# Optimization experiments

Hardware: AMD Instinct MI355X
Metric: run time of the kernel (lower is better)

Reference implementation:

```python
import jax, jax.numpy as jnp
import numpy as np

B, S, D, DF, H, L, K, NT, NM, MAXD = 16, 128, 384, 1536, 2, 6, 3, 128, 80, 8
LOUT = S * MAXD  # fixed (jit-static) upper bound on expanded mel length


def layer_norm(x, g, b):
    m = x.mean(-1, keepdims=True)
    v = x.var(-1, keepdims=True)
    return (x - m) * jax.lax.rsqrt(v + 1e-5) * g + b


def conv1d_same(x, w, b):
    # x: [B,T,Cin], w: [Cout,Cin,K] (torch Conv1d layout), padding='same'
    y = jax.lax.conv_general_dilated(x.transpose(0, 2, 1), w, (1,), 'SAME',
                                     dimension_numbers=('NCH', 'OIH', 'NCH'))
    return y.transpose(0, 2, 1) + b


def self_attention(x, qkv_w, qkv_b, ow, ob):
    b, t, d = x.shape
    dh = d // H
    qkv = x @ qkv_w + qkv_b
    q, k, v = jnp.split(qkv, 3, axis=-1)
    q = q.reshape(b, t, H, dh)
    k = k.reshape(b, t, H, dh)
    v = v.reshape(b, t, H, dh)
    s = jnp.einsum('bqhd,bkhd->bhqk', q, k) / np.sqrt(dh).astype(x.dtype)
    a = jax.nn.softmax(s, axis=-1)
    o = jnp.einsum('bhqk,bkhd->bqhd', a, v).reshape(b, t, d)
    return o @ ow + ob


def fft_block(x, p):
    qkv_w, qkv_b, ow, ob, g1, b1, c1w, c1b, c2w, c2b, g2, b2 = p
    x = layer_norm(x + self_attention(x, qkv_w, qkv_b, ow, ob), g1, b1)
    h = jax.nn.relu(conv1d_same(x, c1w, c1b))
    h = conv1d_same(h, c2w, c2b)
    return layer_norm(x + h, g2, b2)


def pos_encoding(x):
    t, d = x.shape[1], x.shape[2]
    pos = jnp.arange(t, dtype=x.dtype)[:, None]
    i = jnp.arange(d // 2, dtype=x.dtype)[None, :]
    ang = pos / jnp.power(jnp.asarray(10000.0, x.dtype), 2 * i / d)
    pe = jnp.stack([jnp.sin(ang), jnp.cos(ang)], axis=-1).reshape(t, d)
    return x + pe


def fastspeech_fwd(x, y, emb,
                   ph_qkv_w, ph_qkv_b, ph_out_w, ph_out_b, ph_ln1_g, ph_ln1_b,
                   ph_c1_w, ph_c1_b, ph_c2_w, ph_c2_b, ph_ln2_g, ph_ln2_b,
                   mel_qkv_w, mel_qkv_b, mel_out_w, mel_out_b, mel_ln1_g, mel_ln1_b,
                   mel_c1_w, mel_c1_b, mel_c2_w, mel_c2_b, mel_ln2_g, mel_ln2_b,
                   dp_c1_w, dp_c1_b, dp_ln1_g, dp_ln1_b, dp_c2_w, dp_c2_b,
                   dp_ln2_g, dp_ln2_b, dp_lin_w, dp_lin_b,
                   proj_w, proj_b):
    h = emb[x]                      # [B,S,D]
    h = pos_encoding(h)
    ph = (ph_qkv_w, ph_qkv_b, ph_out_w, ph_out_b, ph_ln1_g, ph_ln1_b,
          ph_c1_w, ph_c1_b, ph_c2_w, ph_c2_b, ph_ln2_g, ph_ln2_b)
    for i in range(L):
        h = fft_block(h, tuple(a[i] for a in ph))

    # duration predictor (teacher durations y are used for expansion)
    dp = jax.nn.relu(conv1d_same(h, dp_c1_w, dp_c1_b))
    dp = layer_norm(dp, dp_ln1_g, dp_ln1_b)
    dp = jax.nn.relu(conv1d_same(dp, dp_c2_w, dp_c2_b))
    dp = layer_norm(dp, dp_ln2_g, dp_ln2_b)
    _pred_lengths = (dp @ dp_lin_w + dp_lin_b)[..., 0]  # [B,S] (used only for MSE loss)

    # length regulation: repeat_interleave + pad, vectorized via cumsum+searchsorted
    ends = jnp.cumsum(y, axis=1)                        # [B,S]
    grid = jnp.arange(LOUT)
    idx = jax.vmap(lambda e: jnp.searchsorted(e, grid, side='right'))(ends)  # [B,LOUT]
    idx = jnp.minimum(idx, S - 1)
    mask = grid[None, :] < ends[:, -1:]                 # valid (non-pad) positions
    h = jnp.take_along_axis(h, idx[..., None], axis=1) * mask[..., None]  # [B,LOUT,D]

    mel = (mel_qkv_w, mel_qkv_b, mel_out_w, mel_out_b, mel_ln1_g, mel_ln1_b,
           mel_c1_w, mel_c1_b, mel_c2_w, mel_c2_b, mel_ln2_g, mel_ln2_b)
    for i in range(L):
        h = fft_block(h, tuple(a[i] for a in mel))

    return h @ proj_w + proj_b                          # [B,LOUT,n_mels]


def setup_inputs() -> dict:
    key = jax.random.key(0)
    ks = iter(jax.random.split(key, 64))
    sc = 0.02
    d = {}
    d['x'] = jax.random.randint(next(ks), (B, S), 0, NT, dtype=jnp.int64)
    d['y'] = jax.random.randint(next(ks), (B, S), 1, MAXD + 1, dtype=jnp.int32)
    d['emb'] = jax.random.normal(next(ks), (NT, D), jnp.float32) * sc
    for p in ('ph', 'mel'):
        d[p + '_qkv_w'] = jax.random.normal(next(ks), (L, D, 3 * D), jnp.float32) * sc
        d[p + '_qkv_b'] = jnp.zeros((L, 3 * D), jnp.float32)
        d[p + '_out_w'] = jax.random.normal(next(ks), (L, D, D), jnp.float32) * sc
        d[p + '_out_b'] = jnp.zeros((L, D), jnp.float32)
        d[p + '_ln1_g'] = jnp.ones((L, D), jnp.float32)
        d[p + '_ln1_b'] = jnp.zeros((L, D), jnp.float32)
        d[p + '_c1_w'] = jax.random.normal(next(ks), (L, DF, D, K), jnp.float32) * sc
        d[p + '_c1_b'] = jnp.zeros((L, DF), jnp.float32)
        d[p + '_c2_w'] = jax.random.normal(next(ks), (L, D, DF, K), jnp.float32) * sc
        d[p + '_c2_b'] = jnp.zeros((L, D), jnp.float32)
        d[p + '_ln2_g'] = jnp.ones((L, D), jnp.float32)
        d[p + '_ln2_b'] = jnp.zeros((L, D), jnp.float32)
    d['dp_c1_w'] = jax.random.normal(next(ks), (D, D, K), jnp.float32) * sc
    d['dp_c1_b'] = jnp.zeros((D,), jnp.float32)
    d['dp_ln1_g'] = jnp.ones((D,), jnp.float32)
    d['dp_ln1_b'] = jnp.zeros((D,), jnp.float32)
    d['dp_c2_w'] = jax.random.normal(next(ks), (D, D, K), jnp.float32) * sc
    d['dp_c2_b'] = jnp.zeros((D,), jnp.float32)
    d['dp_ln2_g'] = jnp.ones((D,), jnp.float32)
    d['dp_ln2_b'] = jnp.zeros((D,), jnp.float32)
    d['dp_lin_w'] = jax.random.normal(next(ks), (D, 1), jnp.float32) * sc
    d['dp_lin_b'] = jnp.zeros((1,), jnp.float32)
    d['proj_w'] = jax.random.normal(next(ks), (D, NM), jnp.float32) * sc
    d['proj_b'] = jnp.zeros((NM,), jnp.float32)
    return d


def reference(x, y, emb,
              ph_qkv_w, ph_qkv_b, ph_out_w, ph_out_b, ph_ln1_g, ph_ln1_b,
              ph_c1_w, ph_c1_b, ph_c2_w, ph_c2_b, ph_ln2_g, ph_ln2_b,
              mel_qkv_w, mel_qkv_b, mel_out_w, mel_out_b, mel_ln1_g, mel_ln1_b,
              mel_c1_w, mel_c1_b, mel_c2_w, mel_c2_b, mel_ln2_g, mel_ln2_b,
              dp_c1_w, dp_c1_b, dp_ln1_g, dp_ln1_b, dp_c2_w, dp_c2_b,
              dp_ln2_g, dp_ln2_b, dp_lin_w, dp_lin_b,
              proj_w, proj_b):
    return fastspeech_fwd(x, y, emb,
                          ph_qkv_w, ph_qkv_b, ph_out_w, ph_out_b, ph_ln1_g, ph_ln1_b,
                          ph_c1_w, ph_c1_b, ph_c2_w, ph_c2_b, ph_ln2_g, ph_ln2_b,
                          mel_qkv_w, mel_qkv_b, mel_out_w, mel_out_b, mel_ln1_g, mel_ln1_b,
                          mel_c1_w, mel_c1_b, mel_c2_w, mel_c2_b, mel_ln2_g, mel_ln2_b,
                          dp_c1_w, dp_c1_b, dp_ln1_g, dp_ln1_b, dp_c2_w, dp_c2_b,
                          dp_ln2_g, dp_ln2_b, dp_lin_w, dp_lin_b,
                          proj_w, proj_b)
```

## Files before the change

kernel.cpp:

```cpp
#include <hip/hip_runtime.h>
#include <cstddef>
#include <cmath>

constexpr int CB  = 16;
constexpr int CS  = 128;
constexpr int CD  = 384;
constexpr int CDF = 1536;
constexpr int CH  = 2;
constexpr int CL  = 6;
constexpr int CNM = 80;
constexpr int CLOUT = 1024;
constexpr int CDH = 192;

typedef __bf16 bf16x8 __attribute__((ext_vector_type(8)));
typedef float  f32x4  __attribute__((ext_vector_type(4)));

constexpr int LDT = 72;
__global__ __launch_bounds__(256) void mm_bf16(
    const __bf16* __restrict__ A, long lda, long sA1, long sA2,
    const __bf16* __restrict__ Bt, long ldb, long sB1, long sB2,
    const float* __restrict__ bias, const float* __restrict__ resid,
    void* __restrict__ Cp, long ldc, long sC1, long sC2,
    int M, int N, int K, int zdiv, int relu, int outBf, float scale)
{
    int z = blockIdx.z;
    int zb = z / zdiv, zh = z % zdiv;
    const __bf16* Ab = A  + (long)zb * sA1 + (long)zh * sA2;
    const __bf16* Bb = Bt + (long)zb * sB1 + (long)zh * sB2;
    long coff = (long)zb * sC1 + (long)zh * sC2;

    __shared__ __attribute__((aligned(16))) __bf16 As[128 * LDT];
    __shared__ __attribute__((aligned(16))) __bf16 Bs[128 * LDT];

    int tid  = threadIdx.x;
    int lane = tid & 63;
    int wave = tid >> 6;
    int quad = lane >> 4;
    int l16  = lane & 15;
    int wm = (wave >> 1) * 64;
    int wn = (wave & 1) * 64;

    int mBase = blockIdx.y * 128;
    int nBase = blockIdx.x * 128;

    int trow  = tid >> 3;
    int tcol8 = (tid & 7) * 8;

    f32x4 acc[4][4] = {};

    for (int k0 = 0; k0 < K; k0 += 64) {
#pragma unroll
        for (int p = 0; p < 4; ++p) {
            int r = p * 32 + trow;
            const __bf16* ga = Ab + (long)(mBase + r) * lda + k0 + tcol8;
            *(uint4*)(&As[r * LDT + tcol8]) = *(const uint4*)ga;
            int gn = nBase + r; gn = gn < N ? gn : N - 1;
            const __bf16* gb = Bb + (long)gn * ldb + k0 + tcol8;
            *(uint4*)(&Bs[r * LDT + tcol8]) = *(const uint4*)gb;
        }
        __syncthreads();
#pragma unroll
        for (int ks = 0; ks < 2; ++ks) {
            int kof = ks * 32 + quad * 8;
            bf16x8 af[4], bfr[4];
#pragma unroll
            for (int mt = 0; mt < 4; ++mt)
                af[mt] = *(const bf16x8*)(&As[(wm + mt * 16 + l16) * LDT + kof]);
#pragma unroll
            for (int nt = 0; nt < 4; ++nt)
                bfr[nt] = *(const bf16x8*)(&Bs[(wn + nt * 16 + l16) * LDT + kof]);
#pragma unroll
            for (int mt = 0; mt < 4; ++mt)
#pragma unroll
                for (int nt = 0; nt < 4; ++nt)
                    acc[mt][nt] = __builtin_amdgcn_mfma_f32_16x16x32_bf16(
                        af[mt], bfr[nt], acc[mt][nt], 0, 0, 0);
        }
        __syncthreads();
    }

#pragma unroll
    for (int mt = 0; mt < 4; ++mt) {
#pragma unroll
        for (int nt = 0; nt < 4; ++nt) {
            int col = nBase + wn + nt * 16 + l16;
            if (col >= N) continue;
            int row0 = mBase + wm + mt * 16 + quad * 4;
            float bv = bias ? bias[col] : 0.f;
#pragma unroll
            for (int r = 0; r < 4; ++r) {
                long off = coff + (long)(row0 + r) * ldc + col;
                float v = acc[mt][nt][r] * scale + bv;
                if (resid) v += resid[off];
                if (relu) v = fmaxf(v, 0.f);
                if (outBf) ((__bf16*)Cp)[off] = (__bf16)v;
                else       ((float*)Cp)[off] = v;
            }
        }
    }
}

template<int WN>
__global__ __launch_bounds__(256) void conv_mfma2(
    const __bf16* __restrict__ Apad, const __bf16* __restrict__ W,
    const float* __restrict__ bias, const float* __restrict__ resid,
    void* __restrict__ Cp, long ldc, long sC1,
    int T, int Tp2, int Cc, int O, int relu, int outBf)
{
    constexpr int BN   = 2 * WN;
    constexpr int NT   = WN / 16;
    constexpr int LDT2 = 40;

    int z = blockIdx.z;
    int t0 = blockIdx.y * 128;
    int nBase = blockIdx.x * BN;
    const __bf16* Ab = Apad + ((long)z * Tp2 + t0) * Cc;

    __shared__ __attribute__((aligned(16))) __bf16 As[130 * LDT2];
    __shared__ __attribute__((aligned(16))) __bf16 Bs[3][BN * LDT2];

    int tid  = threadIdx.x;
    int lane = tid & 63;
    int wave = tid >> 6;
    int quad = lane >> 4;
    int l16  = lane & 15;
    int wm = (wave >> 1) * 64;
    int wn = (wave & 1) * WN;

    f32x4 acc[4][NT] = {};

    long ldw = 3L * Cc;
    for (int c0 = 0; c0 < Cc; c0 += 32) {
        __syncthreads();
#pragma unroll
        for (int i = 0; i < 3; ++i) {
            int u = tid + i * 256;
            if (u < 520) {
                int r = u >> 2, cc = (u & 3) * 8;
                *(uint4*)(&As[r * LDT2 + cc]) = *(const uint4*)(Ab + (long)r * Cc + c0 + cc);
            }
        }
#pragma unroll
        for (int i = 0; i < 3 * BN / 64; ++i) {
            int u = tid + i * 256;
            int kk = u / (BN * 4), rr = (u >> 2) & (BN - 1), cc = (u & 3) * 8;
            *(uint4*)(&Bs[kk][rr * LDT2 + cc]) =
                *(const uint4*)(W + (long)(nBase + rr) * ldw + kk * Cc + c0 + cc);
        }
        __syncthreads();
#pragma unroll
        for (int kk = 0; kk < 3; ++kk) {
            bf16x8 a[4], b[NT];
#pragma unroll
            for (int mt = 0; mt < 4; ++mt)
                a[mt] = *(const bf16x8*)(&As[(wm + mt * 16 + l16 + kk) * LDT2 + quad * 8]);
#pragma unroll
            for (int nt = 0; nt < NT; ++nt)
                b[nt] = *(const bf16x8*)(&Bs[kk][(wn + nt * 16 + l16) * LDT2 + quad * 8]);
#pragma unroll
            for (int mt = 0; mt < 4; ++mt)
#pragma unroll
                for (int nt = 0; nt < NT; ++nt)
                    acc[mt][nt] = __builtin_amdgcn_mfma_f32_16x16x32_bf16(
                        a[mt], b[nt], acc[mt][nt], 0, 0, 0);
        }
    }

#pragma unroll
    for (int mt = 0; mt < 4; ++mt) {
#pragma unroll
        for (int nt = 0; nt < NT; ++nt) {
            int col = nBase + wn + nt * 16 + l16;
            int trow = t0 + wm + mt * 16 + quad * 4;
            float bv = bias[col];
#pragma unroll
            for (int r = 0; r < 4; ++r) {
                long off = (long)z * sC1 + (long)(trow + r) * ldc + col;
                float v = acc[mt][nt][r] + bv;
                if (resid) v += resid[off];
                if (relu) v = fmaxf(v, 0.f);
                if (outBf) ((__bf16*)Cp)[off] = (__bf16)v;
                else       ((float*)Cp)[off] = v;
            }
        }
    }
}

__global__ __launch_bounds__(512) void flash_attn(
    const __bf16* __restrict__ qkv, __bf16* __restrict__ o, int T, float scl)
{
    int z = blockIdx.y;
    int b = z >> 1, h = z & 1;
    const __bf16* base = qkv + (long)b * T * 3 * CD + h * CDH;
    int qBase = blockIdx.x * 128;

    __shared__ __attribute__((aligned(16))) __bf16 Qs[128][200];
    __shared__ __attribute__((aligned(16))) __bf16 Ks[64][200];
    __shared__ __attribute__((aligned(16))) __bf16 Vt[192][72];
    __shared__ __attribute__((aligned(16))) __bf16 Ps[128][72];

    int tid  = threadIdx.x;
    int lane = tid & 63;
    int wave = tid >> 6;
    int quad = lane >> 4;
    int l16  = lane & 15;
    int wq   = wave * 16;

#pragma unroll
    for (int i = 0; i < 6; ++i) {
        int u = tid + i * 512;
        int r = u / 24, c = (u % 24) * 8;
        *(uint4*)(&Qs[r][c]) = *(const uint4*)(base + (long)(qBase + r) * 3 * CD + c);
    }

    f32x4 oacc[12];
#pragma unroll
    for (int j = 0; j < 12; ++j) oacc[j] = (f32x4){0.f, 0.f, 0.f, 0.f};
    float mrow[4], lrow[4];
#pragma unroll
    for (int r = 0; r < 4; ++r) { mrow[r] = -3.0e38f; lrow[r] = 0.f; }

    for (int kv0 = 0; kv0 < T; kv0 += 64) {
        __syncthreads();
#pragma unroll
        for (int i = 0; i < 3; ++i) {
            int u = tid + i * 512;
            int r = u / 24, c = (u % 24) * 8;
            *(uint4*)(&Ks[r][c]) = *(const uint4*)(base + CD + (long)(kv0 + r) * 3 * CD + c);
        }
#pragma unroll
        for (int i = 0; i < 3; ++i) {
            int u = tid + i * 512;
            int r = u & 63, c = (u >> 6) * 8;
            uint4 pkt = *(const uint4*)(base + 2 * CD + (long)(kv0 + r) * 3 * CD + c);
            const __bf16* v8 = (const __bf16*)&pkt;
#pragma unroll
            for (int j = 0; j < 8; ++j) Vt[c + j][r] = v8[j];
        }
        __syncthreads();

        f32x4 s[4];
#pragma unroll
        for (int nt = 0; nt < 4; ++nt) s[nt] = (f32x4){0.f, 0.f, 0.f, 0.f};
#pragma unroll
        for (int ks = 0; ks < 6; ++ks) {
            bf16x8 aq = *(const bf16x8*)(&Qs[wq + l16][ks * 32 + quad * 8]);
#pragma unroll
            for (int nt = 0; nt < 4; ++nt) {
                bf16x8 bk = *(const bf16x8*)(&Ks[nt * 16 + l16][ks * 32 + quad * 8]);
                s[nt] = __builtin_amdgcn_mfma_f32_16x16x32_bf16(aq, bk, s[nt], 0, 0, 0);
            }
        }
        float alpha[4];
#pragma unroll
        for (int r = 0; r < 4; ++r) {
            float mx = -3.0e38f;
#pragma unroll
            for (int nt = 0; nt < 4; ++nt) {
                s[nt][r] *= scl;
                mx = fmaxf(mx, s[nt][r]);
            }
            mx = fmaxf(mx, __shfl_xor(mx, 1));
            mx = fmaxf(mx, __shfl_xor(mx, 2));
            mx = fmaxf(mx, __shfl_xor(mx, 4));
            mx = fmaxf(mx, __shfl_xor(mx, 8));
            float mnew = fmaxf(mrow[r], mx);
            alpha[r] = __expf(mrow[r] - mnew);
            mrow[r] = mnew;
            float rs = 0.f;
#pragma unroll
            for (int nt = 0; nt < 4; ++nt) {
                float e = __expf(s[nt][r] - mnew);
                s[nt][r] = e;
                rs += e;
            }
            rs += __shfl_xor(rs, 1);
            rs += __shfl_xor(rs, 2);
            rs += __shfl_xor(rs, 4);
            rs += __shfl_xor(rs, 8);
            lrow[r] = lrow[r] * alpha[r] + rs;
        }
#pragma unroll
        for (int r = 0; r < 4; ++r)
#pragma unroll
            for (int nt = 0; nt < 4; ++nt)
                Ps[wq + quad * 4 + r][nt * 16 + l16] = (__bf16)s[nt][r];
#pragma unroll
        for (int j = 0; j < 12; ++j)
#pragma unroll
            for (int r = 0; r < 4; ++r) oacc[j][r] *= alpha[r];
#pragma unroll
        for (int ks2 = 0; ks2 < 2; ++ks2) {
            bf16x8 ap = *(const bf16x8*)(&Ps[wq + l16][ks2 * 32 + quad * 8]);
#pragma unroll
            for (int nt = 0; nt < 12; ++nt) {
                bf16x8 bv = *(const bf16x8*)(&Vt[nt * 16 + l16][ks2 * 32 + quad * 8]);
                oacc[nt] = __builtin_amdgcn_mfma_f32_16x16x32_bf16(ap, bv, oacc[nt], 0, 0, 0);
            }
        }
    }

    __bf16* ob = o + ((long)b * T + qBase + wq + quad * 4) * CD + h * CDH + l16;
#pragma unroll
    for (int r = 0; r < 4; ++r) {
        float inv = 1.0f / lrow[r];
#pragma unroll
        for (int nt = 0; nt < 12; ++nt)
            ob[(long)r * CD + nt * 16] = (__bf16)(oacc[nt][r] * inv);
    }
}

__global__ __launch_bounds__(CD) void ln_res(const float* __restrict__ a,
    const float* __restrict__ g, const float* __restrict__ be,
    float* __restrict__ out32, __bf16* __restrict__ outbf, int Tlog2)
{
    long r = blockIdx.x;
    int d = threadIdx.x;
    float v = a[r * CD + d];
    float s1 = v, s2 = v * v;
#pragma unroll
    for (int off = 32; off > 0; off >>= 1) {
        s1 += __shfl_down(s1, off);
        s2 += __shfl_down(s2, off);
    }
    __shared__ float sh1[CD / 64], sh2[CD / 64];
    int wv = d >> 6, ln = d & 63;
    if (ln == 0) { sh1[wv] = s1; sh2[wv] = s2; }
    __syncthreads();
    if (d == 0) {
        float t1 = 0.f, t2 = 0.f;
        for (int i = 0; i < CD / 64; ++i) { t1 += sh1[i]; t2 += sh2[i]; }
        sh1[0] = t1; sh2[0] = t2;
    }
    __syncthreads();
    float mean = sh1[0] * (1.0f / CD);
    float var  = sh2[0] * (1.0f / CD) - mean * mean;
    float res = (v - mean) * rsqrtf(var + 1e-5f) * g[d] + be[d];
    out32[r * CD + d] = res;
    int T = 1 << Tlog2;
    long bb = r >> Tlog2; int t = (int)(r & (T - 1));
    outbf[(bb * (T + 2) + t + 1) * CD + d] = (__bf16)res;
}

__global__ __launch_bounds__(CD) void f32_to_padbf16(const float* __restrict__ in,
    __bf16* __restrict__ out, int Tlog2)
{
    long r = blockIdx.x;
    int d = threadIdx.x;
    int T = 1 << Tlog2;
    long b = r >> Tlog2; int t = (int)(r & (T - 1));
    out[(b * (T + 2) + t + 1) * CD + d] = (__bf16)in[r * CD + d];
}

__global__ void zero_pads(__bf16* __restrict__ p, int Tp2, int C)
{
    int b = blockIdx.x >> 1;
    int which = blockIdx.x & 1;
    long row = (long)b * Tp2 + (which ? Tp2 - 1 : 0);
    for (int c = threadIdx.x; c < C; c += blockDim.x) p[row * C + c] = (__bf16)0.f;
}

__global__ __launch_bounds__(256) void tr_f32_bf16(const float* __restrict__ in,
    __bf16* __restrict__ out, int R, int C)
{
    __shared__ float t[32][33];
    int c0 = blockIdx.x * 32, r0 = blockIdx.y * 32;
    int tx = threadIdx.x & 31, ty = threadIdx.x >> 5;
#pragma unroll
    for (int i = 0; i < 4; ++i) {
        int rr = ty * 4 + i;
        int r = r0 + rr, c = c0 + tx;
        if (r < R && c < C) t[rr][tx] = in[(long)r * C + c];
    }
    __syncthreads();
#pragma unroll
    for (int i = 0; i < 4; ++i) {
        int cc = ty * 4 + i;
        int c = c0 + cc, r = r0 + tx;
        if (c < C && r < R) out[(long)c * R + r] = (__bf16)t[tx][cc];
    }
}

__global__ void convw_bf16(const float* __restrict__ w, __bf16* __restrict__ wt,
                           int O, int Cc)
{
    long total = (long)O * 3 * Cc;
    int KC = 3 * Cc;
    for (long i = (long)blockIdx.x * blockDim.x + threadIdx.x; i < total;
         i += (long)gridDim.x * blockDim.x) {
        int j = (int)(i % KC); long o = i / KC;
        int kk = j / Cc, c = j % Cc;
        wt[i] = (__bf16)w[(o * Cc + c) * 3 + kk];
    }
}

__global__ __launch_bounds__(CD) void embed_pe_kernel(const int* __restrict__ x,
    const float* __restrict__ emb, float* __restrict__ h)
{
    int bs = blockIdx.x;
    int d  = threadIdx.x;
    int s  = bs & (CS - 1);
    int tok = x[bs];
    int i = d >> 1;
    float ang = (float)s * powf(10000.0f, -2.0f * (float)i / (float)CD);
    float pe = (d & 1) ? cosf(ang) : sinf(ang);
    h[(size_t)bs * CD + d] = emb[(size_t)tok * CD + d] + pe;
}

__global__ __launch_bounds__(CS) void lenreg_kernel(const int* __restrict__ y,
    int* __restrict__ idx, int* __restrict__ totals)
{
    __shared__ int ends[CS];
    int b = blockIdx.x, tid = threadIdx.x;
    if (tid == 0) {
        int acc = 0;
        for (int s = 0; s < CS; ++s) { acc += y[b * CS + s]; ends[s] = acc; }
    }
    __syncthreads();
    for (int t = tid; t < CLOUT; t += CS) idx[b * CLOUT + t] = CS - 1;
    if (tid == 0) totals[b] = ends[CS - 1];
    __syncthreads();
    int st = (tid == 0) ? 0 : ends[tid - 1];
    int en = ends[tid];
    for (int t = st; t < en; ++t) idx[b * CLOUT + t] = tid;
}

__global__ __launch_bounds__(CD) void gather_dual(const float* __restrict__ hph,
    const int* __restrict__ idx, const int* __restrict__ tot,
    float* __restrict__ h32, __bf16* __restrict__ hbf, int chunkBase)
{
    int rl = blockIdx.x;
    int rg = chunkBase + rl;
    int b = rg >> 10, t = rg & (CLOUT - 1);
    int d = threadIdx.x;
    int src = idx[rg];
    float v = (t < tot[b]) ? hph[((long)b * CS + src) * CD + d] : 0.f;
    h32[(long)rl * CD + d] = v;
    long bl = rl >> 10; int tl = rl & (CLOUT - 1);
    hbf[(bl * (CLOUT + 2) + tl + 1) * CD + d] = (__bf16)v;
}


static inline void mm(hipStream_t st, const __bf16* A, long lda, long sA1, long sA2,
    const __bf16* Bt, long ldb, long sB1, long sB2, const float* bias,
    const float* resid, void* C, long ldc, long sC1, long sC2, int M, int N, int K,
    int nz, int zdiv, int relu, int outBf, float scale)
{
    dim3 g((N + 127) / 128, M / 128, nz), b(256, 1, 1);
    hipLaunchKernelGGL(mm_bf16, g, b, 0, st, A, lda, sA1, sA2, Bt, ldb, sB1, sB2,
                       bias, resid, C, ldc, sC1, sC2, M, N, K, zdiv, relu, outBf, scale);
}

struct Scr {
    float *h32, *x32, *tmp32;
    __bf16 *hbf, *xbf, *qkv, *c1p, *o;
};

static size_t scr_layout(char* base, int NB, int T, Scr* s)
{
    auto align = [](size_t v) { return (v + 255) & ~(size_t)255; };
    size_t off = 0;
    long Tp2 = T + 2;
    if (s) s->h32 = (float*)(base + off);
    off = align(off + (size_t)NB * T * CD * 4);
    if (s) s->x32 = (float*)(base + off);
    off = align(off + (size_t)NB * T * CD * 4);
    if (s) s->tmp32 = (float*)(base + off);
    off = align(off + (size_t)NB * T * CD * 4);
    if (s) s->hbf = (__bf16*)(base + off);
    off = align(off + (size_t)NB * Tp2 * CD * 2);
    if (s) s->xbf = (__bf16*)(base + off);
    off = align(off + (size_t)NB * Tp2 * CD * 2);
    if (s) s->qkv = (__bf16*)(base + off);
    off = align(off + (size_t)NB * T * 3 * CD * 2);
    if (s) s->c1p = (__bf16*)(base + off);
    off = align(off + (size_t)NB * Tp2 * CDF * 2);
    if (s) s->o = (__bf16*)(base + off);
    off = align(off + (size_t)NB * T * CD * 2);
    return off;
}

constexpr long W_QKV = 0;
constexpr long W_OUT = 442368;
constexpr long W_C1  = 589824;
constexpr long W_C2  = 2359296;
constexpr long WLAYER = 4128768;
constexpr long WSTACK = 6 * WLAYER;
constexpr long WTOT   = WSTACK + 30720;

static void convert_stack_weights(hipStream_t st, __bf16* wbuf,
    const float* qkv_w, const float* out_w, const float* c1w, const float* c2w)
{
    for (int l = 0; l < CL; ++l) {
        __bf16* wl = wbuf + (long)l * WLAYER;
        hipLaunchKernelGGL(tr_f32_bf16, dim3(36, 12), dim3(256), 0, st,
                           qkv_w + (long)l * CD * 3 * CD, wl + W_QKV, CD, 3 * CD);
        hipLaunchKernelGGL(tr_f32_bf16, dim3(12, 12), dim3(256), 0, st,
                           out_w + (long)l * CD * CD, wl + W_OUT, CD, CD);
        hipLaunchKernelGGL(convw_bf16, dim3(2048), dim3(256), 0, st,
                           c1w + (long)l * CDF * CD * 3, wl + W_C1, CDF, CD);
        hipLaunchKernelGGL(convw_bf16, dim3(2048), dim3(256), 0, st,
                           c2w + (long)l * CD * CDF * 3, wl + W_C2, CD, CDF);
    }
}

static void fft_block_bf16(hipStream_t st, const Scr& S, int NBc, int T, int tlog2,
    float* h32, const __bf16* wl,
    const float* qkv_b, const float* out_b,
    const float* g1, const float* b1, const float* c1b, const float* c2b,
    const float* g2, const float* b2)
{
    const int M = NBc * T;
    const long Tp2 = T + 2;
    const float scl = 1.0f / sqrtf((float)CDH);

    mm(st, S.hbf + CD, CD, Tp2 * CD, 0, wl + W_QKV, CD, 0, 0, qkv_b, nullptr,
       S.qkv, 3 * CD, (long)T * 3 * CD, 0, T, 3 * CD, CD, NBc, 1, 0, 1, 1.f);

    hipLaunchKernelGGL(flash_attn, dim3(T / 128, NBc * CH), dim3(512), 0, st,
                       S.qkv, S.o, T, scl);

    mm(st, S.o, CD, 0, 0, wl + W_OUT, CD, 0, 0, out_b, h32,
       S.tmp32, CD, 0, 0, M, CD, CD, 1, 1, 0, 0, 1.f);

    hipLaunchKernelGGL(ln_res, dim3(M), dim3(CD), 0, st,
                       S.tmp32, g1, b1, S.x32, S.xbf, tlog2);

    hipLaunchKernelGGL((conv_mfma2<128>), dim3(CDF / 256, T / 128, NBc), dim3(256), 0, st,
                       S.xbf, wl + W_C1, c1b, nullptr,
                       (void*)(S.c1p + CDF), (long)CDF, Tp2 * CDF,
                       T, (int)Tp2, CD, CDF, 1, 1);

    hipLaunchKernelGGL((conv_mfma2<64>), dim3(CD / 128, T / 128, NBc), dim3(256), 0, st,
                       S.c1p, wl + W_C2, c2b, S.x32,
                       S.tmp32, (long)CD, (long)T * CD,
                       T, (int)Tp2, CDF, CD, 0, 0);

    hipLaunchKernelGGL(ln_res, dim3(M), dim3(CD), 0, st,
                       S.tmp32, g2, b2, h32, S.hbf, tlog2);
}

extern "C" void kernel_launch(void* const* d_in, const int* in_sizes, int n_in,
                              void* d_out, int out_size, void* d_ws, size_t ws_size,
                              hipStream_t stream)
{
    (void)in_sizes; (void)out_size;

    const int* x = (const int*)d_in[0];
    const int* y = (const int*)d_in[1];
    const float* P[40];
    for (int i = 0; i < n_in && i < 40; ++i) P[i] = (const float*)d_in[i];

    size_t wbufB  = ((size_t)WTOT * 2 + 255) & ~(size_t)255;
    size_t hphB   = ((size_t)CB * CS * CD * 4 + 255) & ~(size_t)255;
    size_t idxB   = (((size_t)CB * CLOUT + CB) * 4 + 255) & ~(size_t)255;
    size_t fixedB = wbufB + hphB + idxB;

    size_t scrB = (ws_size > fixedB) ? (ws_size - fixedB) : 0;

    int NBmel = 1;
    for (int cand = 16; cand >= 1; cand >>= 1)
        if (scr_layout(nullptr, cand, CLOUT, nullptr) <= scrB) { NBmel = cand; break; }

    int NBph = 1;
    for (int cand = 16; cand >= 1; cand >>= 1)
        if (scr_layout(nullptr, cand, CS, nullptr) <= scrB) { NBph = cand; break; }

    char* base = (char*)d_ws;
    __bf16* wbuf = (__bf16*)base;
    float*  hPh  = (float*)(base + wbufB);
    int*    idxb = (int*)(base + wbufB + hphB);
    int*    totb = idxb + (long)CB * CLOUT;
    char*   scrbase = base + fixedB;

    convert_stack_weights(stream, wbuf, P[3], P[5], P[9], P[11]);

    Scr Sp; scr_layout(scrbase, NBph, CS, &Sp);
    hipLaunchKernelGGL(zero_pads, dim3(NBph * 2), dim3(256), 0, stream, Sp.hbf, CS + 2, CD);
    hipLaunchKernelGGL(zero_pads, dim3(NBph * 2), dim3(256), 0, stream, Sp.xbf, CS + 2, CD);
    hipLaunchKernelGGL(zero_pads, dim3(NBph * 2), dim3(256), 0, stream, Sp.c1p, CS + 2, CDF);

    hipLaunchKernelGGL(embed_pe_kernel, dim3(CB * CS), dim3(CD), 0, stream, x, P[2], hPh);

    for (int c = 0; c < CB / NBph; ++c) {
        float* hch = hPh + (long)c * NBph * CS * CD;
        hipLaunchKernelGGL(f32_to_padbf16, dim3(NBph * CS), dim3(CD), 0, stream,
                           hch, Sp.hbf, 7);
        for (int l = 0; l < CL; ++l)
            fft_block_bf16(stream, Sp, NBph, CS, 7, hch, wbuf + (long)l * WLAYER,
                           P[4] + (long)l * 3 * CD, P[6] + (long)l * CD,
                           P[7] + (long)l * CD, P[8] + (long)l * CD,
                           P[10] + (long)l * CDF, P[12] + (long)l * CD,
                           P[13] + (long)l * CD, P[14] + (long)l * CD);
    }

    hipLaunchKernelGGL(lenreg_kernel, dim3(CB), dim3(CS), 0, stream, y, idxb, totb);

    convert_stack_weights(stream, wbuf, P[15], P[17], P[21], P[23]);
    hipLaunchKernelGGL(tr_f32_bf16, dim3(3, 12), dim3(256), 0, stream,
                       P[37], wbuf + WSTACK, CD, CNM);

    Scr Sm; scr_layout(scrbase, NBmel, CLOUT, &Sm);
    hipLaunchKernelGGL(zero_pads, dim3(NBmel * 2), dim3(256), 0, stream, Sm.hbf, CLOUT + 2, CD);
    hipLaunchKernelGGL(zero_pads, dim3(NBmel * 2), dim3(256), 0, stream, Sm.xbf, CLOUT + 2, CD);
    hipLaunchKernelGGL(zero_pads, dim3(NBmel * 2), dim3(256), 0, stream, Sm.c1p, CLOUT + 2, CDF);

    for (int c = 0; c < CB / NBmel; ++c) {
        hipLaunchKernelGGL(gather_dual, dim3(NBmel * CLOUT), dim3(CD), 0, stream,
                           hPh, idxb, totb, Sm.h32, Sm.hbf, c * NBmel * CLOUT);
        for (int l = 0; l < CL; ++l)
            fft_block_bf16(stream, Sm, NBmel, CLOUT, 10, Sm.h32, wbuf + (long)l * WLAYER,
                           P[16] + (long)l * 3 * CD, P[18] + (long)l * CD,
                           P[19] + (long)l * CD, P[20] + (long)l * CD,
                           P[22] + (long)l * CDF, P[24] + (long)l * CD,
                           P[25] + (long)l * CD, P[26] + (long)l * CD);
        mm(stream, Sm.hbf + CD, CD, (long)(CLOUT + 2) * CD, 0,
           wbuf + WSTACK, CD, 0, 0, P[38], nullptr,
           (float*)d_out + (long)c * NBmel * CLOUT * CNM, CNM, (long)CLOUT * CNM, 0,
           CLOUT, CNM, CD, NBmel, 1, 0, 0, 1.f);
    }
}
```

Baseline: 4.353 ms.

## Prefetch conv tiles into registers and use 512-thread blocks in conv kernel

The conv MFMA kernel now uses 8 waves (512 threads) per block, with each wave covering half as many output columns, so the tile size per block is unchanged. Global loads for the next K-chunk are issued into registers before the current chunk's MFMAs run, then written to shared memory at the start of the next iteration. The aim is to hide global memory latency behind compute and raise the number of waves per CU. In exchange each thread holds extra prefetch registers and does a smaller MFMA tile, which lowers per-wave operand reuse.

New measurement: 6.036 ms. +38.7%, slower.

```diff
diff --git a/kernel.cpp b/kernel.cpp
--- a/kernel.cpp
+++ b/kernel.cpp
@@ -101,15 +101,16 @@
 }
 
 template<int WN>
-__global__ __launch_bounds__(256) void conv_mfma2(
+__global__ __launch_bounds__(512) void conv_mfma3(
     const __bf16* __restrict__ Apad, const __bf16* __restrict__ W,
     const float* __restrict__ bias, const float* __restrict__ resid,
     void* __restrict__ Cp, long ldc, long sC1,
     int T, int Tp2, int Cc, int O, int relu, int outBf)
 {
-    constexpr int BN   = 2 * WN;
-    constexpr int NT   = WN / 16;
-    constexpr int LDT2 = 40;
+    constexpr int BN    = 4 * WN;
+    constexpr int NT    = WN / 16;
+    constexpr int LDT2  = 40;
+    constexpr int BITER = 3 * BN * 4 / 512;
 
     int z = blockIdx.z;
     int t0 = blockIdx.y * 128;
@@ -124,30 +125,65 @@
     int wave = tid >> 6;
     int quad = lane >> 4;
     int l16  = lane & 15;
-    int wm = (wave >> 1) * 64;
-    int wn = (wave & 1) * WN;
+    int wm = (wave >> 2) * 64;
+    int wn = (wave & 3) * WN;
 
     f32x4 acc[4][NT] = {};
 
     long ldw = 3L * Cc;
+
+    uint4 aR[2];
+    uint4 bR[BITER];
+
+    auto loadA = [&](int c0) {
+#pragma unroll
+        for (int i = 0; i < 2; ++i) {
+            int u = tid + i * 512;
+            if (u < 520) {
+                int r = u >> 2, cc = (u & 3) * 8;
+                aR[i] = *(const uint4*)(Ab + (long)r * Cc + c0 + cc);
+            }
+        }
+    };
+    auto loadB = [&](int c0) {
+#pragma unroll
+        for (int i = 0; i < BITER; ++i) {
+            int u = tid + i * 512;
+            int kk = u / (BN * 4), rr = (u >> 2) & (BN - 1), cc = (u & 3) * 8;
+            bR[i] = *(const uint4*)(W + (long)(nBase + rr) * ldw + kk * Cc + c0 + cc);
+        }
+    };
+    auto storeA = [&]() {
+#pragma unroll
+        for (int i = 0; i < 2; ++i) {
+            int u = tid + i * 512;
+            if (u < 520) {
+                int r = u >> 2, cc = (u & 3) * 8;
+                *(uint4*)(&As[r * LDT2 + cc]) = aR[i];
+            }
+        }
+    };
+    auto storeB = [&]() {
+#pragma unroll
+        for (int i = 0; i < BITER; ++i) {
+            int u = tid + i * 512;
+            int kk = u / (BN * 4), rr = (u >> 2) & (BN - 1), cc = (u & 3) * 8;
+            *(uint4*)(&Bs[kk][rr * LDT2 + cc]) = bR[i];
+        }
+    };
+
+    loadA(0);
+    loadB(0);
+
     for (int c0 = 0; c0 < Cc; c0 += 32) {
         __syncthreads();
-#pragma unroll
-        for (int i = 0; i < 3; ++i) {
-            int u = tid + i * 256;
-            if (u < 520) {
-                int r = u >> 2, cc = (u & 3) * 8;
-                *(uint4*)(&As[r * LDT2 + cc]) = *(const uint4*)(Ab + (long)r * Cc + c0 + cc);
-            }
-        }
-#pragma unroll
-        for (int i = 0; i < 3 * BN / 64; ++i) {
-            int u = tid + i * 256;
-            int kk = u / (BN * 4), rr = (u >> 2) & (BN - 1), cc = (u & 3) * 8;
-            *(uint4*)(&Bs[kk][rr * LDT2 + cc]) =
-                *(const uint4*)(W + (long)(nBase + rr) * ldw + kk * Cc + c0 + cc);
-        }
+        storeA();
+        storeB();
         __syncthreads();
+        if (c0 + 32 < Cc) {
+            loadA(c0 + 32);
+            loadB(c0 + 32);
+        }
 #pragma unroll
         for (int kk = 0; kk < 3; ++kk) {
             bf16x8 a[4], b[NT];
@@ -526,12 +562,12 @@
     hipLaunchKernelGGL(ln_res, dim3(M), dim3(CD), 0, st,
                        S.tmp32, g1, b1, S.x32, S.xbf, tlog2);
 
-    hipLaunchKernelGGL((conv_mfma2<128>), dim3(CDF / 256, T / 128, NBc), dim3(256), 0, st,
+    hipLaunchKernelGGL((conv_mfma3<64>), dim3(CDF / 256, T / 128, NBc), dim3(512), 0, st,
                        S.xbf, wl + W_C1, c1b, nullptr,
                        (void*)(S.c1p + CDF), (long)CDF, Tp2 * CDF,
                        T, (int)Tp2, CD, CDF, 1, 1);
 
-    hipLaunchKernelGGL((conv_mfma2<64>), dim3(CD / 128, T / 128, NBc), dim3(256), 0, st,
+    hipLaunchKernelGGL((conv_mfma3<32>), dim3(CD / 128, T / 128, NBc), dim3(512), 0, st,
                        S.c1p, wl + W_C2, c2b, S.x32,
                        S.tmp32, (long)CD, (long)T * CD,
                        T, (int)Tp2, CDF, CD, 0, 0);
```
